# Optimization experiments

Hardware: AMD Instinct MI355X
Metric: run time of the kernel (lower is better)

The kernel has to match this reference:

```python
import jax, jax.numpy as jnp
import numpy as np

N_NODES = 100000
N_EDGES = 3200000


def gcn_conv(x, src, dst, W, b, n):
    # GCNConv with self-loops and symmetric deg^-1/2 normalization (PyG defaults)
    loop = jnp.arange(n)
    s = jnp.concatenate([src, loop])
    d = jnp.concatenate([dst, loop])
    deg = jax.ops.segment_sum(jnp.ones_like(s, dtype=x.dtype), d, num_segments=n)
    dinv = jnp.where(deg > 0, jax.lax.rsqrt(deg), 0.0)
    norm = dinv[s] * dinv[d]                      # [E+N]
    h = x @ W.T                                   # [N, out]
    msgs = h[s] * norm[:, None]                   # gather + scale
    return jax.ops.segment_sum(msgs, d, num_segments=n) + b


def setup_inputs() -> dict:
    key = jax.random.key(0)
    k = jax.random.split(key, 6)
    x = jax.random.normal(k[0], (N_NODES, 64), dtype=jnp.float32)
    edge_index = jax.random.randint(k[1], (2, N_EDGES), 0, N_NODES, dtype=jnp.int64)
    # glorot-ish init for GCNConv linear weights, zero bias (PyG default bias init is zeros)
    W1 = jax.random.normal(k[2], (32, 64), dtype=jnp.float32) * (1.0 / np.sqrt(64))
    b1 = jnp.zeros((32,), dtype=jnp.float32)
    W2 = jax.random.normal(k[3], (16, 32), dtype=jnp.float32) * (1.0 / np.sqrt(32))
    b2 = jnp.zeros((16,), dtype=jnp.float32)
    return {"x": x, "edge_index": edge_index, "W1": W1, "b1": b1, "W2": W2, "b2": b2}


def reference(x, edge_index, W1, b1, W2, b2):
    n = x.shape[0]
    src, dst = edge_index[0], edge_index[1]
    # encode (eval mode: dropout is identity)
    h = jax.nn.relu(gcn_conv(x, src, dst, W1, b1, n))
    z = gcn_conv(h, src, dst, W2, b2, n)          # [N, 16]
    # decode: edge-wise dot product + sigmoid
    return jax.nn.sigmoid(jnp.sum(z[src] * z[dst], axis=-1))  # [E]
```

## Files before the change

kernel.cpp:

```cpp
#include <hip/hip_runtime.h>
#include <hip/hip_fp16.h>
#include <math.h>

#define NN 100000
#define NE 3200000
#define NB 391
#define CH 4096
#define NPART ((NE + CH - 1) / CH)

__device__ inline float2 u2f2(unsigned v) {
    __half2 h = *reinterpret_cast<__half2*>(&v);
    return __half22float2(h);
}

__global__ void bhist_kernel(const int* __restrict__ dst, int* __restrict__ bhist, int e) {
    __shared__ int h[NB];
    int tid = threadIdx.x;
    for (int i = tid; i < NB; i += 256) h[i] = 0;
    __syncthreads();
    for (int i = blockIdx.x * blockDim.x + tid; i < e; i += gridDim.x * blockDim.x)
        atomicAdd(&h[dst[i] >> 8], 1);
    __syncthreads();
    for (int i = tid; i < NB; i += 256) if (h[i]) atomicAdd(&bhist[i], h[i]);
}

__global__ void bscan_kernel(const int* __restrict__ bhist, int* __restrict__ boffs,
                             int* __restrict__ cursor) {
    __shared__ int s[512];
    int tid = threadIdx.x;
    int v = (tid < NB) ? bhist[tid] : 0;
    s[tid] = v;
    __syncthreads();
    for (int off = 1; off < 512; off <<= 1) {
        int t = (tid >= off) ? s[tid - off] : 0;
        __syncthreads();
        s[tid] += t;
        __syncthreads();
    }
    if (tid < NB) {
        int ex = s[tid] - v;
        boffs[tid] = ex;
        cursor[tid] = ex;
    }
}

__global__ __launch_bounds__(256) void partition_kernel(
        const int* __restrict__ src, const int* __restrict__ dst,
        int* __restrict__ cursor, int* __restrict__ adj, int e) {
    __shared__ int scnt[NB];
    __shared__ int sbase[NB];
    __shared__ int lexcl[NB];
    __shared__ int sA[512], sB[512];
    __shared__ int sdata[CH];
    __shared__ unsigned short srank[CH];
    __shared__ unsigned short pbuk[CH];

    int tid = threadIdx.x;
    int chunk0 = blockIdx.x * CH;
    int cnt = e - chunk0; if (cnt > CH) cnt = CH;

    for (int i = tid; i < NB; i += 256) scnt[i] = 0;
    __syncthreads();

    for (int k = 0; k < CH / 256; ++k) {
        int li = k * 256 + tid;
        int i = chunk0 + li;
        if (i < e) {
            int b = dst[i] >> 8;
            int r = atomicAdd(&scnt[b], 1);
            srank[li] = (unsigned short)r;
        }
    }
    __syncthreads();

    for (int b = tid; b < NB; b += 256)
        if (scnt[b]) sbase[b] = atomicAdd(&cursor[b], scnt[b]);

    {
        int* pa = sA; int* pb = sB;
        pa[tid]       = (tid < NB) ? scnt[tid] : 0;
        pa[tid + 256] = (tid + 256 < NB) ? scnt[tid + 256] : 0;
        __syncthreads();
        for (int off = 1; off < 512; off <<= 1) {
            for (int q = tid; q < 512; q += 256)
                pb[q] = pa[q] + ((q >= off) ? pa[q - off] : 0);
            __syncthreads();
            int* t = pa; pa = pb; pb = t;
        }
        if (tid < NB)       lexcl[tid]       = pa[tid]       - scnt[tid];
        if (tid + 256 < NB) lexcl[tid + 256] = pa[tid + 256] - scnt[tid + 256];
    }
    __syncthreads();

    for (int k = 0; k < CH / 256; ++k) {
        int li = k * 256 + tid;
        int i = chunk0 + li;
        if (i < e) {
            int s = src[i], d = dst[i];
            int b = d >> 8;
            int p = lexcl[b] + (int)srank[li];
            sdata[p] = (s << 8) | (d & 255);
            pbuk[p] = (unsigned short)b;
        }
    }
    __syncthreads();

    for (int p = tid; p < cnt; p += 256) {
        int b = pbuk[p];
        adj[sbase[b] + (p - lexcl[b])] = sdata[p];
    }
}

__global__ __launch_bounds__(256) void csr_kernel(
        const int* __restrict__ bhist, const int* __restrict__ boffs,
        const int* __restrict__ adj, int* __restrict__ adj2,
        int* __restrict__ rowptr, float* __restrict__ dinv, int n) {
    __shared__ int cnt[256];
    __shared__ int s[256];
    __shared__ int cur[256];
    int tid = threadIdx.x;
    int b = blockIdx.x;
    cnt[tid] = 0;
    __syncthreads();
    int ebeg = boffs[b], ecnt = bhist[b];
    for (int j = tid; j < ecnt; j += 256)
        atomicAdd(&cnt[adj[ebeg + j] & 255], 1);
    __syncthreads();
    int v = cnt[tid];
    s[tid] = v;
    __syncthreads();
    for (int off = 1; off < 256; off <<= 1) {
        int t = (tid >= off) ? s[tid - off] : 0;
        __syncthreads();
        s[tid] += t;
        __syncthreads();
    }
    int excl = s[tid] - v;
    cur[tid] = excl;
    int node = b * 256 + tid;
    if (node < n) {
        rowptr[node] = ebeg + excl;
        dinv[node] = rsqrtf((float)v + 1.0f);
    }
    if (node == n) rowptr[n] = ebeg + excl;
    __syncthreads();
    for (int j = tid; j < ecnt; j += 256) {
        int w = adj[ebeg + j];
        int p = atomicAdd(&cur[w & 255], 1);
        adj2[ebeg + p] = w >> 8;
    }
}

__global__ __launch_bounds__(256) void gemm1_kernel(
        const float* __restrict__ x, const float* __restrict__ W1,
        const float* __restrict__ dinv, __half* __restrict__ g1a,
        __half* __restrict__ g1b, int n) {
    __shared__ float sW[64 * 32];
    __shared__ float sX[32 * 65];
    int tid = threadIdx.x;
    for (int idx = tid; idx < 2048; idx += 256) {
        int k = idx >> 5, c = idx & 31;
        sW[idx] = W1[c * 64 + k];
    }
    int row0 = blockIdx.x * 32;
    for (int idx = tid; idx < 512; idx += 256) {
        int r = idx >> 4, q = idx & 15;
        int grow = row0 + r;
        float4 v = (grow < n) ? ((const float4*)x)[(size_t)grow * 16 + q]
                              : make_float4(0.f, 0.f, 0.f, 0.f);
        float* dp = &sX[r * 65 + q * 4];
        dp[0] = v.x; dp[1] = v.y; dp[2] = v.z; dp[3] = v.w;
    }
    __syncthreads();
    int r = tid >> 3, cg = tid & 7;
    const float4* sW4 = (const float4*)sW;
    float4 acc = make_float4(0.f, 0.f, 0.f, 0.f);
#pragma unroll
    for (int k = 0; k < 64; ++k) {
        float xk = sX[r * 65 + k];
        float4 w = sW4[k * 8 + cg];
        acc.x += xk * w.x; acc.y += xk * w.y; acc.z += xk * w.z; acc.w += xk * w.w;
    }
    int grow = row0 + r;
    if (grow < n) {
        float di = dinv[grow];
        __half2 h0 = __float22half2_rn(make_float2(acc.x * di, acc.y * di));
        __half2 h1 = __float22half2_rn(make_float2(acc.z * di, acc.w * di));
        uint2 packed;
        packed.x = *(unsigned*)&h0;
        packed.y = *(unsigned*)&h1;
        if (cg < 4) ((uint2*)g1a)[(size_t)grow * 4 + cg] = packed;
        else        ((uint2*)g1b)[(size_t)grow * 4 + (cg - 4)] = packed;
    }
}

__global__ __launch_bounds__(256) void agg1_kernel(
        const int* __restrict__ rowptr, const int* __restrict__ adj2,
        const float* __restrict__ dinv, const __half* __restrict__ gh,
        const float* __restrict__ b1, float* __restrict__ agg1, int n, int pass) {
    int t = blockIdx.x * blockDim.x + threadIdx.x;
    int node = t >> 3;
    if (node >= n) return;
    int c2 = t & 7;
    const unsigned* G = (const unsigned*)gh;
    float2 acc = u2f2(G[(size_t)node * 8 + c2]);
    int j = rowptr[node], end = rowptr[node + 1];
    for (; j + 3 < end; j += 4) {
        int s0 = adj2[j], s1 = adj2[j + 1], s2 = adj2[j + 2], s3 = adj2[j + 3];
        float2 v0 = u2f2(G[(size_t)s0 * 8 + c2]);
        float2 v1 = u2f2(G[(size_t)s1 * 8 + c2]);
        float2 v2 = u2f2(G[(size_t)s2 * 8 + c2]);
        float2 v3 = u2f2(G[(size_t)s3 * 8 + c2]);
        acc.x += (v0.x + v1.x) + (v2.x + v3.x);
        acc.y += (v0.y + v1.y) + (v2.y + v3.y);
    }
    for (; j < end; ++j) {
        float2 v = u2f2(G[(size_t)adj2[j] * 8 + c2]);
        acc.x += v.x; acc.y += v.y;
    }
    float di = dinv[node];
    float2 bb = ((const float2*)b1)[pass * 8 + c2];
    float2 outv = make_float2(bb.x + di * acc.x, bb.y + di * acc.y);
    ((float2*)agg1)[(size_t)node * 16 + pass * 8 + c2] = outv;
}

__global__ __launch_bounds__(256) void gemm2_kernel(
        const float* __restrict__ agg1, const float* __restrict__ W2,
        const float* __restrict__ dinv, __half* __restrict__ g2h, int n) {
    __shared__ float sW[32 * 16];
    __shared__ float sH[64 * 33];
    int tid = threadIdx.x;
    for (int idx = tid; idx < 512; idx += 256) {
        int k = idx >> 4, c = idx & 15;
        sW[idx] = W2[c * 32 + k];
    }
    int row0 = blockIdx.x * 64;
    for (int idx = tid; idx < 512; idx += 256) {
        int r = idx >> 3, q = idx & 7;
        int grow = row0 + r;
        float4 v = (grow < n) ? ((const float4*)agg1)[(size_t)grow * 8 + q]
                              : make_float4(0.f, 0.f, 0.f, 0.f);
        float* dp = &sH[r * 33 + q * 4];
        dp[0] = fmaxf(v.x, 0.f); dp[1] = fmaxf(v.y, 0.f);
        dp[2] = fmaxf(v.z, 0.f); dp[3] = fmaxf(v.w, 0.f);
    }
    __syncthreads();
    int r = tid >> 2, cg = tid & 3;
    const float4* sW4 = (const float4*)sW;
    float4 acc = make_float4(0.f, 0.f, 0.f, 0.f);
#pragma unroll
    for (int k = 0; k < 32; ++k) {
        float hk = sH[r * 33 + k];
        float4 w = sW4[k * 4 + cg];
        acc.x += hk * w.x; acc.y += hk * w.y; acc.z += hk * w.z; acc.w += hk * w.w;
    }
    int grow = row0 + r;
    if (grow < n) {
        float di = dinv[grow];
        __half2 h0 = __float22half2_rn(make_float2(acc.x * di, acc.y * di));
        __half2 h1 = __float22half2_rn(make_float2(acc.z * di, acc.w * di));
        uint2 packed;
        packed.x = *(unsigned*)&h0;
        packed.y = *(unsigned*)&h1;
        ((uint2*)g2h)[(size_t)grow * 4 + cg] = packed;
    }
}

__global__ __launch_bounds__(256) void agg2_kernel(
        const int* __restrict__ rowptr, const int* __restrict__ adj2,
        const float* __restrict__ dinv, const __half* __restrict__ g2h,
        const float* __restrict__ b2, __half* __restrict__ zh, int n) {
    int t = blockIdx.x * blockDim.x + threadIdx.x;
    int node = t >> 3;
    if (node >= n) return;
    int c2 = t & 7;
    const unsigned* G = (const unsigned*)g2h;
    float2 acc = u2f2(G[(size_t)node * 8 + c2]);
    int j = rowptr[node], end = rowptr[node + 1];
    for (; j + 3 < end; j += 4) {
        int s0 = adj2[j], s1 = adj2[j + 1], s2 = adj2[j + 2], s3 = adj2[j + 3];
        float2 v0 = u2f2(G[(size_t)s0 * 8 + c2]);
        float2 v1 = u2f2(G[(size_t)s1 * 8 + c2]);
        float2 v2 = u2f2(G[(size_t)s2 * 8 + c2]);
        float2 v3 = u2f2(G[(size_t)s3 * 8 + c2]);
        acc.x += (v0.x + v1.x) + (v2.x + v3.x);
        acc.y += (v0.y + v1.y) + (v2.y + v3.y);
    }
    for (; j < end; ++j) {
        float2 v = u2f2(G[(size_t)adj2[j] * 8 + c2]);
        acc.x += v.x; acc.y += v.y;
    }
    float di = dinv[node];
    float2 bb = ((const float2*)b2)[c2];
    __half2 outv = __float22half2_rn(make_float2(bb.x + di * acc.x, bb.y + di * acc.y));
    ((__half2*)zh)[(size_t)node * 8 + c2] = outv;
}

__device__ inline float dot2u(unsigned a, unsigned b) {
    float2 fa = u2f2(a), fb = u2f2(b);
    return fa.x * fb.x + fa.y * fb.y;
}

__global__ void decode_kernel(const int* __restrict__ src, const int* __restrict__ dst,
                              const __half* __restrict__ zh, float* __restrict__ out, int e) {
    int i = blockIdx.x * blockDim.x + threadIdx.x;
    if (i < e) {
        int s = src[i], d = dst[i];
        const uint4* Zs = (const uint4*)(zh + (size_t)s * 16);
        const uint4* Zd = (const uint4*)(zh + (size_t)d * 16);
        uint4 a0 = Zs[0], a1 = Zs[1];
        uint4 b0 = Zd[0], b1 = Zd[1];
        float acc = dot2u(a0.x, b0.x) + dot2u(a0.y, b0.y)
                  + dot2u(a0.z, b0.z) + dot2u(a0.w, b0.w)
                  + dot2u(a1.x, b1.x) + dot2u(a1.y, b1.y)
                  + dot2u(a1.z, b1.z) + dot2u(a1.w, b1.w);
        out[i] = 1.0f / (1.0f + expf(-acc));
    }
}

extern "C" void kernel_launch(void* const* d_in, const int* in_sizes, int n_in,
                              void* d_out, int out_size, void* d_ws, size_t ws_size,
                              hipStream_t stream) {
    const float* x   = (const float*)d_in[0];
    const int* eidx  = (const int*)d_in[1];
    const float* W1  = (const float*)d_in[2];
    const float* b1  = (const float*)d_in[3];
    const float* W2  = (const float*)d_in[4];
    const float* b2  = (const float*)d_in[5];
    float* out = (float*)d_out;

    const int n = NN;
    const int e = NE;
    const int* src = eidx;
    const int* dst = eidx + e;

    int* bhist   = (int*)d_ws;
    int* boffs   = bhist + 512;
    int* cursor  = boffs + 512;
    int* rowptr  = cursor + 512;
    int* adj     = rowptr + 100004;
    int* adj2    = adj + e;
    float* dinv  = (float*)(adj2 + e);
    __half* g1a  = (__half*)adj;
    __half* g1b  = g1a + (size_t)n * 16;
    float* agg1  = dinv + n;
    __half* g2h  = (__half*)(agg1 + (size_t)n * 32);
    __half* zh   = g2h + (size_t)n * 16;

    dim3 blk(256);

    hipMemsetAsync(bhist, 0, 512 * sizeof(int), stream);
    bhist_kernel<<<1024, blk, 0, stream>>>(dst, bhist, e);
    bscan_kernel<<<1, 512, 0, stream>>>(bhist, boffs, cursor);
    partition_kernel<<<NPART, blk, 0, stream>>>(src, dst, cursor, adj, e);
    csr_kernel<<<NB, blk, 0, stream>>>(bhist, boffs, adj, adj2, rowptr, dinv, n);

    gemm1_kernel<<<(n + 31) / 32, blk, 0, stream>>>(x, W1, dinv, g1a, g1b, n);
    agg1_kernel<<<(n * 8 + 255) / 256, blk, 0, stream>>>(rowptr, adj2, dinv, g1a, b1, agg1, n, 0);
    agg1_kernel<<<(n * 8 + 255) / 256, blk, 0, stream>>>(rowptr, adj2, dinv, g1b, b1, agg1, n, 1);

    gemm2_kernel<<<(n + 63) / 64, blk, 0, stream>>>(agg1, W2, dinv, g2h, n);
    agg2_kernel<<<(n * 8 + 255) / 256, blk, 0, stream>>>(rowptr, adj2, dinv, g2h, b2, zh, n);

    decode_kernel<<<(e + 255) / 256, blk, 0, stream>>>(src, dst, zh, out, e);
}
```

Before: 272.0 us.

## Use nontemporal memory ops, widen CSR blocks, and process two edges per decode thread

Streaming loads and stores across the pipeline are replaced with nontemporal builtins to reduce cache pollution. The CSR build kernel now runs 1024-thread blocks, and the partition chunk size is halved to give more blocks. The decode kernel handles two edges per thread using 64-bit index loads and a packed output store. The risk is that nontemporal hints on data that is reused later (adj2, zh, agg1) could cause cache misses.

```diff
diff --git a/kernel.cpp b/kernel.cpp
--- a/kernel.cpp
+++ b/kernel.cpp
@@ -5,8 +5,11 @@
 #define NN 100000
 #define NE 3200000
 #define NB 391
-#define CH 4096
+#define CH 2048
 #define NPART ((NE + CH - 1) / CH)
+
+typedef float f32x4 __attribute__((ext_vector_type(4)));
+typedef unsigned long long u64;
 
 __device__ inline float2 u2f2(unsigned v) {
     __half2 h = *reinterpret_cast<__half2*>(&v);
@@ -19,7 +22,7 @@
     for (int i = tid; i < NB; i += 256) h[i] = 0;
     __syncthreads();
     for (int i = blockIdx.x * blockDim.x + tid; i < e; i += gridDim.x * blockDim.x)
-        atomicAdd(&h[dst[i] >> 8], 1);
+        atomicAdd(&h[__builtin_nontemporal_load(&dst[i]) >> 8], 1);
     __syncthreads();
     for (int i = tid; i < NB; i += 256) if (h[i]) atomicAdd(&bhist[i], h[i]);
 }
@@ -66,7 +69,7 @@
         int li = k * 256 + tid;
         int i = chunk0 + li;
         if (i < e) {
-            int b = dst[i] >> 8;
+            int b = __builtin_nontemporal_load(&dst[i]) >> 8;
             int r = atomicAdd(&scnt[b], 1);
             srank[li] = (unsigned short)r;
         }
@@ -96,7 +99,8 @@
         int li = k * 256 + tid;
         int i = chunk0 + li;
         if (i < e) {
-            int s = src[i], d = dst[i];
+            int s = __builtin_nontemporal_load(&src[i]);
+            int d = __builtin_nontemporal_load(&dst[i]);
             int b = d >> 8;
             int p = lexcl[b] + (int)srank[li];
             sdata[p] = (s << 8) | (d & 255);
@@ -107,11 +111,11 @@
 
     for (int p = tid; p < cnt; p += 256) {
         int b = pbuk[p];
-        adj[sbase[b] + (p - lexcl[b])] = sdata[p];
-    }
-}
-
-__global__ __launch_bounds__(256) void csr_kernel(
+        __builtin_nontemporal_store(sdata[p], &adj[sbase[b] + (p - lexcl[b])]);
+    }
+}
+
+__global__ __launch_bounds__(1024) void csr_kernel(
         const int* __restrict__ bhist, const int* __restrict__ boffs,
         const int* __restrict__ adj, int* __restrict__ adj2,
         int* __restrict__ rowptr, float* __restrict__ dinv, int n) {
@@ -120,34 +124,37 @@
     __shared__ int cur[256];
     int tid = threadIdx.x;
     int b = blockIdx.x;
-    cnt[tid] = 0;
+    if (tid < 256) cnt[tid] = 0;
     __syncthreads();
     int ebeg = boffs[b], ecnt = bhist[b];
-    for (int j = tid; j < ecnt; j += 256)
-        atomicAdd(&cnt[adj[ebeg + j] & 255], 1);
-    __syncthreads();
-    int v = cnt[tid];
-    s[tid] = v;
+    for (int j = tid; j < ecnt; j += 1024)
+        atomicAdd(&cnt[__builtin_nontemporal_load(&adj[ebeg + j]) & 255], 1);
+    __syncthreads();
+    int v = 0;
+    if (tid < 256) { v = cnt[tid]; s[tid] = v; }
     __syncthreads();
     for (int off = 1; off < 256; off <<= 1) {
-        int t = (tid >= off) ? s[tid - off] : 0;
-        __syncthreads();
-        s[tid] += t;
-        __syncthreads();
-    }
-    int excl = s[tid] - v;
-    cur[tid] = excl;
-    int node = b * 256 + tid;
-    if (node < n) {
-        rowptr[node] = ebeg + excl;
-        dinv[node] = rsqrtf((float)v + 1.0f);
-    }
-    if (node == n) rowptr[n] = ebeg + excl;
-    __syncthreads();
-    for (int j = tid; j < ecnt; j += 256) {
-        int w = adj[ebeg + j];
+        int t = 0;
+        if (tid < 256 && tid >= off) t = s[tid - off];
+        __syncthreads();
+        if (tid < 256) s[tid] += t;
+        __syncthreads();
+    }
+    if (tid < 256) {
+        int excl = s[tid] - v;
+        cur[tid] = excl;
+        int node = b * 256 + tid;
+        if (node < n) {
+            rowptr[node] = ebeg + excl;
+            dinv[node] = rsqrtf((float)v + 1.0f);
+        }
+        if (node == n) rowptr[n] = ebeg + excl;
+    }
+    __syncthreads();
+    for (int j = tid; j < ecnt; j += 1024) {
+        int w = __builtin_nontemporal_load(&adj[ebeg + j]);
         int p = atomicAdd(&cur[w & 255], 1);
-        adj2[ebeg + p] = w >> 8;
+        __builtin_nontemporal_store(w >> 8, &adj2[ebeg + p]);
     }
 }
 
@@ -166,8 +173,8 @@
     for (int idx = tid; idx < 512; idx += 256) {
         int r = idx >> 4, q = idx & 15;
         int grow = row0 + r;
-        float4 v = (grow < n) ? ((const float4*)x)[(size_t)grow * 16 + q]
-                              : make_float4(0.f, 0.f, 0.f, 0.f);
+        f32x4 v = (f32x4)(0.f);
+        if (grow < n) v = __builtin_nontemporal_load((const f32x4*)x + (size_t)grow * 16 + q);
         float* dp = &sX[r * 65 + q * 4];
         dp[0] = v.x; dp[1] = v.y; dp[2] = v.z; dp[3] = v.w;
     }
@@ -206,7 +213,10 @@
     float2 acc = u2f2(G[(size_t)node * 8 + c2]);
     int j = rowptr[node], end = rowptr[node + 1];
     for (; j + 3 < end; j += 4) {
-        int s0 = adj2[j], s1 = adj2[j + 1], s2 = adj2[j + 2], s3 = adj2[j + 3];
+        int s0 = __builtin_nontemporal_load(&adj2[j]);
+        int s1 = __builtin_nontemporal_load(&adj2[j + 1]);
+        int s2 = __builtin_nontemporal_load(&adj2[j + 2]);
+        int s3 = __builtin_nontemporal_load(&adj2[j + 3]);
         float2 v0 = u2f2(G[(size_t)s0 * 8 + c2]);
         float2 v1 = u2f2(G[(size_t)s1 * 8 + c2]);
         float2 v2 = u2f2(G[(size_t)s2 * 8 + c2]);
@@ -215,13 +225,14 @@
         acc.y += (v0.y + v1.y) + (v2.y + v3.y);
     }
     for (; j < end; ++j) {
-        float2 v = u2f2(G[(size_t)adj2[j] * 8 + c2]);
+        float2 v = u2f2(G[(size_t)__builtin_nontemporal_load(&adj2[j]) * 8 + c2]);
         acc.x += v.x; acc.y += v.y;
     }
     float di = dinv[node];
     float2 bb = ((const float2*)b1)[pass * 8 + c2];
-    float2 outv = make_float2(bb.x + di * acc.x, bb.y + di * acc.y);
-    ((float2*)agg1)[(size_t)node * 16 + pass * 8 + c2] = outv;
+    float ox = bb.x + di * acc.x, oy = bb.y + di * acc.y;
+    u64 pk = ((u64)__float_as_uint(oy) << 32) | __float_as_uint(ox);
+    __builtin_nontemporal_store(pk, (u64*)agg1 + (size_t)node * 16 + pass * 8 + c2);
 }
 
 __global__ __launch_bounds__(256) void gemm2_kernel(
@@ -238,8 +249,8 @@
     for (int idx = tid; idx < 512; idx += 256) {
         int r = idx >> 3, q = idx & 7;
         int grow = row0 + r;
-        float4 v = (grow < n) ? ((const float4*)agg1)[(size_t)grow * 8 + q]
-                              : make_float4(0.f, 0.f, 0.f, 0.f);
+        f32x4 v = (f32x4)(0.f);
+        if (grow < n) v = __builtin_nontemporal_load((const f32x4*)agg1 + (size_t)grow * 8 + q);
         float* dp = &sH[r * 33 + q * 4];
         dp[0] = fmaxf(v.x, 0.f); dp[1] = fmaxf(v.y, 0.f);
         dp[2] = fmaxf(v.z, 0.f); dp[3] = fmaxf(v.w, 0.f);
@@ -278,7 +289,10 @@
     float2 acc = u2f2(G[(size_t)node * 8 + c2]);
     int j = rowptr[node], end = rowptr[node + 1];
     for (; j + 3 < end; j += 4) {
-        int s0 = adj2[j], s1 = adj2[j + 1], s2 = adj2[j + 2], s3 = adj2[j + 3];
+        int s0 = __builtin_nontemporal_load(&adj2[j]);
+        int s1 = __builtin_nontemporal_load(&adj2[j + 1]);
+        int s2 = __builtin_nontemporal_load(&adj2[j + 2]);
+        int s3 = __builtin_nontemporal_load(&adj2[j + 3]);
         float2 v0 = u2f2(G[(size_t)s0 * 8 + c2]);
         float2 v1 = u2f2(G[(size_t)s1 * 8 + c2]);
         float2 v2 = u2f2(G[(size_t)s2 * 8 + c2]);
@@ -287,13 +301,13 @@
         acc.y += (v0.y + v1.y) + (v2.y + v3.y);
     }
     for (; j < end; ++j) {
-        float2 v = u2f2(G[(size_t)adj2[j] * 8 + c2]);
+        float2 v = u2f2(G[(size_t)__builtin_nontemporal_load(&adj2[j]) * 8 + c2]);
         acc.x += v.x; acc.y += v.y;
     }
     float di = dinv[node];
     float2 bb = ((const float2*)b2)[c2];
     __half2 outv = __float22half2_rn(make_float2(bb.x + di * acc.x, bb.y + di * acc.y));
-    ((__half2*)zh)[(size_t)node * 8 + c2] = outv;
+    __builtin_nontemporal_store(*(unsigned*)&outv, (unsigned*)zh + (size_t)node * 8 + c2);
 }
 
 __device__ inline float dot2u(unsigned a, unsigned b) {
@@ -301,20 +315,33 @@
     return fa.x * fb.x + fa.y * fb.y;
 }
 
-__global__ void decode_kernel(const int* __restrict__ src, const int* __restrict__ dst,
-                              const __half* __restrict__ zh, float* __restrict__ out, int e) {
+__device__ inline float edge_dot(const __half* zh, int s, int d) {
+    const uint4* Zs = (const uint4*)(zh + (size_t)s * 16);
+    const uint4* Zd = (const uint4*)(zh + (size_t)d * 16);
+    uint4 a0 = Zs[0], a1 = Zs[1];
+    uint4 b0 = Zd[0], b1 = Zd[1];
+    return dot2u(a0.x, b0.x) + dot2u(a0.y, b0.y)
+         + dot2u(a0.z, b0.z) + dot2u(a0.w, b0.w)
+         + dot2u(a1.x, b1.x) + dot2u(a1.y, b1.y)
+         + dot2u(a1.z, b1.z) + dot2u(a1.w, b1.w);
+}
+
+__global__ __launch_bounds__(256) void decode_kernel(
+        const int* __restrict__ src, const int* __restrict__ dst,
+        const __half* __restrict__ zh, float* __restrict__ out, int e) {
     int i = blockIdx.x * blockDim.x + threadIdx.x;
-    if (i < e) {
-        int s = src[i], d = dst[i];
-        const uint4* Zs = (const uint4*)(zh + (size_t)s * 16);
-        const uint4* Zd = (const uint4*)(zh + (size_t)d * 16);
-        uint4 a0 = Zs[0], a1 = Zs[1];
-        uint4 b0 = Zd[0], b1 = Zd[1];
-        float acc = dot2u(a0.x, b0.x) + dot2u(a0.y, b0.y)
-                  + dot2u(a0.z, b0.z) + dot2u(a0.w, b0.w)
-                  + dot2u(a1.x, b1.x) + dot2u(a1.y, b1.y)
-                  + dot2u(a1.z, b1.z) + dot2u(a1.w, b1.w);
-        out[i] = 1.0f / (1.0f + expf(-acc));
+    int np = e >> 1;
+    if (i < np) {
+        u64 sv = __builtin_nontemporal_load((const u64*)src + i);
+        u64 dv = __builtin_nontemporal_load((const u64*)dst + i);
+        int s0 = (int)(unsigned)sv, s1 = (int)(sv >> 32);
+        int d0 = (int)(unsigned)dv, d1 = (int)(dv >> 32);
+        float acc0 = edge_dot(zh, s0, d0);
+        float acc1 = edge_dot(zh, s1, d1);
+        float o0 = 1.0f / (1.0f + expf(-acc0));
+        float o1 = 1.0f / (1.0f + expf(-acc1));
+        u64 po = ((u64)__float_as_uint(o1) << 32) | __float_as_uint(o0);
+        __builtin_nontemporal_store(po, (u64*)out + i);
     }
 }
 
@@ -353,7 +380,7 @@
     bhist_kernel<<<1024, blk, 0, stream>>>(dst, bhist, e);
     bscan_kernel<<<1, 512, 0, stream>>>(bhist, boffs, cursor);
     partition_kernel<<<NPART, blk, 0, stream>>>(src, dst, cursor, adj, e);
-    csr_kernel<<<NB, blk, 0, stream>>>(bhist, boffs, adj, adj2, rowptr, dinv, n);
+    csr_kernel<<<NB, 1024, 0, stream>>>(bhist, boffs, adj, adj2, rowptr, dinv, n);
 
     gemm1_kernel<<<(n + 31) / 32, blk, 0, stream>>>(x, W1, dinv, g1a, g1b, n);
     agg1_kernel<<<(n * 8 + 255) / 256, blk, 0, stream>>>(rowptr, adj2, dinv, g1a, b1, agg1, n, 0);
@@ -362,5 +389,5 @@
     gemm2_kernel<<<(n + 63) / 64, blk, 0, stream>>>(agg1, W2, dinv, g2h, n);
     agg2_kernel<<<(n * 8 + 255) / 256, blk, 0, stream>>>(rowptr, adj2, dinv, g2h, b2, zh, n);
 
-    decode_kernel<<<(e + 255) / 256, blk, 0, stream>>>(src, dst, zh, out, e);
-}
+    decode_kernel<<<((e / 2) + 255) / 256, blk, 0, stream>>>(src, dst, zh, out, e);
+}
```

Measured after the change: 433.0 us. 59.2% more time.
